# Performance work log

Measured on AMD Instinct MI355X. Metric: run time of the kernel, lower is better.

## Reference

```python
import jax, jax.numpy as jnp
import numpy as np

N_EMBD = 1024
N_HEAD = 16
HEAD_DIM = N_EMBD // N_HEAD


def setup_inputs() -> dict:
    key = jax.random.key(0)
    kx, kq, kk, kv, kp = jax.random.split(key, 5)
    B, S = 4, 2048
    x = jax.random.normal(kx, (B, S, N_EMBD), dtype=jnp.float32)
    # nn.Linear(n, n, bias=False): weight [out, in], y = x @ W.T
    s = 1.0 / np.sqrt(N_EMBD)
    Wq = jax.random.uniform(kq, (N_EMBD, N_EMBD), jnp.float32, -s, s)
    Wk = jax.random.uniform(kk, (N_EMBD, N_EMBD), jnp.float32, -s, s)
    Wv = jax.random.uniform(kv, (N_EMBD, N_EMBD), jnp.float32, -s, s)
    Wo = jax.random.uniform(kp, (N_EMBD, N_EMBD), jnp.float32, -s, s)
    return {"x": x, "Wq": Wq, "Wk": Wk, "Wv": Wv, "Wo": Wo}


def _split_heads(t):
    B, S, _ = t.shape
    return t.reshape(B, S, N_HEAD, HEAD_DIM).transpose(0, 2, 1, 3)  # [B,H,S,D]


def reference(x, Wq, Wk, Wv, Wo):
    q = _split_heads(x @ Wq.T)
    k = _split_heads(x @ Wk.T)
    v = _split_heads(x @ Wv.T)
    scale = 1.0 / np.sqrt(HEAD_DIM)
    scores = jnp.einsum('bhqd,bhkd->bhqk', q, k) * scale  # [B,H,S,S]
    S = x.shape[1]
    mask = jnp.tril(jnp.ones((S, S), dtype=bool))
    masked = jnp.where(mask[None, None], scores, -jnp.inf)
    attn = jax.nn.softmax(masked, axis=-1)
    heads = jnp.einsum('bhqk,bhkd->bhqd', attn, v)
    merged = heads.transpose(0, 2, 1, 3).reshape(x.shape[0], S, N_EMBD)
    return merged @ Wo.T
```

## Files before the change

### kernel.cpp

```cpp
#include <hip/hip_runtime.h>
#include <hip/hip_bf16.h>

typedef __hip_bfloat16 bf16;
typedef __attribute__((ext_vector_type(8))) short short8;
typedef __attribute__((ext_vector_type(4))) float f32x4;
typedef unsigned int uint32;

#define MFMA16(a, b, c) __builtin_amdgcn_mfma_f32_16x16x32_bf16(a, b, c, 0, 0, 0)

constexpr int EMB   = 1024;
constexpr int SEQ   = 2048;
constexpr int BATCH = 4;
constexpr int NH    = 16;
constexpr int HD    = 64;
constexpr int QKVW  = 3 * EMB;
constexpr float QSCALE = 0.125f * 1.44269504f;

__device__ __forceinline__ void gl_lds16(const bf16* g, bf16* l) {
    __builtin_amdgcn_global_load_lds(
        (const __attribute__((address_space(1))) void*)g,
        (__attribute__((address_space(3))) void*)l,
        16, 0, 0);
}

__device__ __forceinline__ float fexp2(float x) {
#if __has_builtin(__builtin_amdgcn_exp2f)
    return __builtin_amdgcn_exp2f(x);
#else
    return exp2f(x);
#endif
}

__device__ __forceinline__ uint32 pack2(float a, float b) {
    uint32 ua = __builtin_bit_cast(uint32, a) + 0x8000u;
    uint32 ub = __builtin_bit_cast(uint32, b) + 0x8000u;
    return __builtin_amdgcn_perm(ub, ua, 0x07060302u);
}

__device__ __forceinline__ bf16 fbf16(float f) {
    unsigned short u =
        (unsigned short)((__builtin_bit_cast(uint32, f) + 0x8000u) >> 16);
    return __builtin_bit_cast(bf16, u);
}

__device__ __forceinline__ int ps_dw(int row, int cd) {
    return row * 64 + ((((cd >> 2) ^ (row & 7)) << 3) + ((cd & 3) << 1));
}

__global__ void convert_all(const float* __restrict__ x,
                            const float* __restrict__ wq,
                            const float* __restrict__ wk,
                            const float* __restrict__ wv,
                            const float* __restrict__ wo,
                            bf16* __restrict__ xc,
                            bf16* __restrict__ wqkv,
                            bf16* __restrict__ woc) {
    const int NX = BATCH * SEQ * EMB;
    const int NW = EMB * EMB;
    const float* src; bf16* dst; int n4, b0, nb;
    const int blk = blockIdx.x;
    if (blk < 2048)      { src = x;  dst = xc;          n4 = NX / 4; b0 = 0;    nb = 2048; }
    else if (blk < 2304) { src = wq; dst = wqkv;        n4 = NW / 4; b0 = 2048; nb = 256; }
    else if (blk < 2560) { src = wk; dst = wqkv + NW;   n4 = NW / 4; b0 = 2304; nb = 256; }
    else if (blk < 2816) { src = wv; dst = wqkv + 2*NW; n4 = NW / 4; b0 = 2560; nb = 256; }
    else                 { src = wo; dst = woc;         n4 = NW / 4; b0 = 2816; nb = 256; }
    for (int i = (blk - b0) * 256 + threadIdx.x; i < n4; i += nb * 256) {
        float4 v = ((const float4*)src)[i];
        uint2 o;
        o.x = pack2(v.x, v.y);
        o.y = pack2(v.z, v.w);
        ((uint2*)dst)[i] = o;
    }
}

template <typename OutT>
__global__ __launch_bounds__(256) void gemm_bt(const bf16* __restrict__ A,
                                               const bf16* __restrict__ B,
                                               OutT* __restrict__ C,
                                               int M, int N, int K,
                                               float oscale, int qlim) {
    __shared__ __align__(16) bf16 As[128 * 64];
    __shared__ __align__(16) bf16 Bs[128 * 64];

    const int t    = threadIdx.x;
    const int lane = t & 63;
    const int wid  = t >> 6;
    const int l16  = lane & 15;
    const int quad = lane >> 4;
    const int e    = l16 & 7;
    const int wm   = (wid >> 1) * 64;
    const int wn   = (wid & 1) * 64;

    const int nwg = (int)gridDim.x;
    const int cpx = nwg >> 3;
    const int wg  = ((int)blockIdx.x & 7) * cpx + ((int)blockIdx.x >> 3);
    const int gx  = N >> 7;
    const int m0  = (wg / gx) * 128;
    const int n0  = (wg % gx) * 128;
    const float sc = (n0 < qlim) ? oscale : 1.0f;

    f32x4 acc[4][4] = {};
    const int srow = lane >> 3;
    const int scol = ((lane & 7) ^ srow) * 8;

    for (int k0 = 0; k0 < K; k0 += 64) {
        #pragma unroll
        for (int it = 0; it < 4; ++it) {
            int rb = it * 32 + wid * 8;
            gl_lds16(&A[(size_t)(m0 + rb + srow) * K + k0 + scol], &As[rb * 64]);
            gl_lds16(&B[(size_t)(n0 + rb + srow) * K + k0 + scol], &Bs[rb * 64]);
        }
        __syncthreads();
        #pragma unroll
        for (int ks = 0; ks < 64; ks += 32) {
            const int cb = (ks >> 3) + quad;
            short8 af[4], bfr[4];
            #pragma unroll
            for (int i = 0; i < 4; ++i)
                af[i] = *(const short8*)&As[(wm + i * 16 + l16) * 64 + ((cb ^ e) * 8)];
            #pragma unroll
            for (int j = 0; j < 4; ++j)
                bfr[j] = *(const short8*)&Bs[(wn + j * 16 + l16) * 64 + ((cb ^ e) * 8)];
            #pragma unroll
            for (int i = 0; i < 4; ++i)
                #pragma unroll
                for (int j = 0; j < 4; ++j)
                    acc[i][j] = MFMA16(af[i], bfr[j], acc[i][j]);
        }
        __syncthreads();
    }

    #pragma unroll
    for (int i = 0; i < 4; ++i)
        #pragma unroll
        for (int j = 0; j < 4; ++j)
            #pragma unroll
            for (int r = 0; r < 4; ++r) {
                int row = m0 + wm + i * 16 + quad * 4 + r;
                int col = n0 + wn + j * 16 + l16;
                float v = acc[i][j][r] * sc;
                if constexpr (sizeof(OutT) == 2)
                    C[(size_t)row * N + col] = fbf16(v);
                else
                    C[(size_t)row * N + col] = (OutT)v;
            }
}

__global__ __launch_bounds__(256) void transpose_v(const bf16* __restrict__ QKV,
                                                   bf16* __restrict__ Vt) {
    __shared__ __align__(16) bf16 Ts[4096];
    const int t  = threadIdx.x;
    const int st = blockIdx.x;
    const int bh = blockIdx.y;
    const int b  = bh >> 4, h = bh & 15;
    const int s0 = st * 64;

    const bf16* src = QKV + ((size_t)(b * SEQ + s0)) * QKVW + 2 * EMB + h * HD;
    {
        int r = t >> 3, cq = t & 7;
        #pragma unroll
        for (int it = 0; it < 2; ++it, r += 32) {
            uint4 v = *(const uint4*)&src[(size_t)r * QKVW + cq * 8];
            int blk = cq ^ (r >> 3);
            *(uint4*)&Ts[r * 64 + blk * 8] = v;
        }
    }
    __syncthreads();
    bf16* dst = Vt + (size_t)bh * HD * SEQ + s0;
    {
        int d = t >> 3;
        const int sq = t & 7;
        #pragma unroll
        for (int it = 0; it < 2; ++it, d += 32) {
            short8 ov;
            #pragma unroll
            for (int i = 0; i < 8; ++i) {
                int s = sq * 8 + i;
                ov[i] = (short)__bfloat16_as_ushort(
                    Ts[s * 64 + (((d >> 3) ^ sq) << 3) + (d & 7)]);
            }
            *(short8*)&dst[(size_t)d * SEQ + sq * 8] = ov;
        }
    }
}

__global__ __launch_bounds__(256) void flash_attn(const bf16* __restrict__ QKV,
                                                  const bf16* __restrict__ Vt,
                                                  bf16* __restrict__ O) {
    __shared__ __align__(16) bf16 Ks[2][64 * 64];
    __shared__ __align__(16) bf16 VTs[2][64 * 64];
    __shared__ __align__(16) bf16 Ps[4][16 * 64];

    const int t    = threadIdx.x;
    const int lane = t & 63;
    const int w    = t >> 6;
    const int l16  = lane & 15;
    const int quad = lane >> 4;
    const int e    = l16 & 7;

    const int lin = (int)blockIdx.x;
    const int wg  = ((lin & 7) << 7) + (lin >> 3);
    const int bh  = wg >> 4;
    const int pr  = wg & 15;
    const int b   = bh >> 4, h = bh & 15;

    const bf16* Qp = QKV + (size_t)b * SEQ * QKVW + h * HD;
    const bf16* Kp = QKV + (size_t)b * SEQ * QKVW + EMB + h * HD;
    const bf16* Vp = Vt + (size_t)bh * HD * SEQ;
    bf16* Op = O + (size_t)b * SEQ * EMB + h * HD;

    const int srow = lane >> 3;
    const int scol = ((lane & 7) ^ srow) * 8;

    auto stage = [&](int kt, int buf) {
        const int kbase = kt * 64;
        #pragma unroll
        for (int it = 0; it < 2; ++it) {
            int rb = it * 32 + w * 8;
            gl_lds16(&Kp[(size_t)(kbase + rb + srow) * QKVW + scol], &Ks[buf][rb * 64]);
            gl_lds16(&Vp[(size_t)(rb + srow) * SEQ + kbase + scol], &VTs[buf][rb * 64]);
        }
    };

    for (int pass = 0; pass < 2; ++pass) {
        const int qt = pass ? pr : 31 - pr;
        const int q0 = qt * 64;
        const int wq0 = q0 + w * 16;

        short8 bQ[2];
        {
            const size_t qr = (size_t)(wq0 + l16) * QKVW;
            bQ[0] = *(const short8*)&Qp[qr + quad * 8];
            bQ[1] = *(const short8*)&Qp[qr + 32 + quad * 8];
        }

        f32x4 o[4] = {};
        float lrow = 0.f;

        const int ntiles = qt + 1;

        stage(0, 0);
        if (ntiles > 1) stage(1, 1);

        for (int kt = 0; kt < ntiles; ++kt) {
            const int cur = kt & 1;
            const int kbase = kt * 64;
            if (kt < ntiles - 1) __builtin_amdgcn_s_waitcnt(0x0F74);
            else                 __builtin_amdgcn_s_waitcnt(0x0F70);
            __builtin_amdgcn_s_barrier();

            f32x4 sa[4];
            #pragma unroll
            for (int j = 0; j < 4; ++j) {
                f32x4 acc = {};
                acc = MFMA16(*(const short8*)&Ks[cur][(j * 16 + l16) * 64 + ((quad ^ e) * 8)],
                             bQ[0], acc);
                acc = MFMA16(*(const short8*)&Ks[cur][(j * 16 + l16) * 64 + (((4 + quad) ^ e) * 8)],
                             bQ[1], acc);
                sa[j] = acc;
            }

            float lsum = 0.f;
            if (kbase + 63 > wq0) {
                #pragma unroll
                for (int j = 0; j < 4; ++j)
                    #pragma unroll
                    for (int pp = 0; pp < 2; ++pp) {
                        int kg = kbase + j * 16 + quad * 4 + 2 * pp;
                        float e0 = fexp2(sa[j][2 * pp]);
                        float e1 = fexp2(sa[j][2 * pp + 1]);
                        float p0 = (kg     <= wq0 + l16) ? e0 : 0.f;
                        float p1 = (kg + 1 <= wq0 + l16) ? e1 : 0.f;
                        lsum += p0 + p1;
                        *(uint32*)&Ps[w][ps_dw(l16, j * 8 + quad * 2 + pp)] = pack2(p0, p1);
                    }
            } else {
                #pragma unroll
                for (int j = 0; j < 4; ++j)
                    #pragma unroll
                    for (int pp = 0; pp < 2; ++pp) {
                        float p0 = fexp2(sa[j][2 * pp]);
                        float p1 = fexp2(sa[j][2 * pp + 1]);
                        lsum += p0 + p1;
                        *(uint32*)&Ps[w][ps_dw(l16, j * 8 + quad * 2 + pp)] = pack2(p0, p1);
                    }
            }
            lrow += lsum;

            #pragma unroll
            for (int ks = 0; ks < 2; ++ks) {
                short8 bP = *(const short8*)&Ps[w][l16 * 64 + (((ks * 4 + quad) ^ e) << 3)];
                #pragma unroll
                for (int dg = 0; dg < 4; ++dg)
                    o[dg] = MFMA16(
                        *(const short8*)&VTs[cur][(dg * 16 + l16) * 64 + (((ks * 4 + quad) ^ e) * 8)],
                        bP, o[dg]);
            }

            __builtin_amdgcn_s_barrier();
            if (kt + 2 < ntiles) stage(kt + 2, cur);
        }

        {
            float l = lrow;
            l += __shfl_xor(l, 16);
            l += __shfl_xor(l, 32);
            float rl = 1.0f / l;
            #pragma unroll
            for (int dg = 0; dg < 4; ++dg)
                #pragma unroll
                for (int pp = 0; pp < 2; ++pp) {
                    float v0 = o[dg][2 * pp] * rl;
                    float v1 = o[dg][2 * pp + 1] * rl;
                    *(uint32*)&Ps[w][ps_dw(l16, dg * 8 + quad * 2 + pp)] = pack2(v0, v1);
                }
            #pragma unroll
            for (int it = 0; it < 2; ++it) {
                int qr = lane >> 2;
                int ch = (lane & 3) + 4 * it;
                short8 vv = *(const short8*)&Ps[w][qr * 64 + ((ch ^ (qr & 7)) << 3)];
                *(short8*)&Op[(size_t)(wq0 + qr) * EMB + ch * 8] = vv;
            }
        }
    }
}

extern "C" void kernel_launch(void* const* d_in, const int* in_sizes, int n_in,
                              void* d_out, int out_size, void* d_ws, size_t ws_size,
                              hipStream_t stream) {
    const float* x  = (const float*)d_in[0];
    const float* Wq = (const float*)d_in[1];
    const float* Wk = (const float*)d_in[2];
    const float* Wv = (const float*)d_in[3];
    const float* Wo = (const float*)d_in[4];
    float* out = (float*)d_out;
    bf16*  ws  = (bf16*)d_ws;

    const int M  = BATCH * SEQ;
    const int NX = M * EMB;
    const int NW = EMB * EMB;

    bf16* xc   = ws;
    bf16* Ab   = xc;
    bf16* Wqkv = ws + (size_t)NX;
    bf16* Woc  = Wqkv + 3 * (size_t)NW;
    bf16* QKV  = Woc + NW;
    bf16* Vt   = QKV + (size_t)M * QKVW;

    convert_all<<<3072, 256, 0, stream>>>(x, Wq, Wk, Wv, Wo, xc, Wqkv, Woc);

    gemm_bt<bf16><<<dim3((QKVW / 128) * (M / 128)), 256, 0, stream>>>(
        xc, Wqkv, QKV, M, QKVW, EMB, QSCALE, EMB);

    transpose_v<<<dim3(SEQ / 64, BATCH * NH), 256, 0, stream>>>(QKV, Vt);

    flash_attn<<<dim3((SEQ / 64 / 2) * BATCH * NH), 256, 0, stream>>>(QKV, Vt, Ab);

    gemm_bt<float><<<dim3((EMB / 128) * (M / 128)), 256, 0, stream>>>(
        Ab, Woc, out, M, EMB, EMB, 1.0f, 0);
}
```

Baseline: 257.3 us.

## Double-buffer GEMM LDS tiles with async global-to-LDS prefetch and XCD tile remap

The bf16 GEMM now keeps two LDS buffers for A and B. It prefetches the tile two steps ahead with global_load_lds, using explicit vmcnt waits and barriers in place of __syncthreads, so loads overlap with the MFMA work. It also changes how workgroups map to tiles: each XCD gets a contiguous band of M rows and walks N tiles, aiming for better L2 reuse. The cost is double the LDS use (64KB), which may lower occupancy, plus reliance on hand-encoded waitcnt values being correct.

```diff
diff --git a/kernel.cpp b/kernel.cpp
--- a/kernel.cpp
+++ b/kernel.cpp
@@ -79,8 +79,8 @@
                                                OutT* __restrict__ C,
                                                int M, int N, int K,
                                                float oscale, int qlim) {
-    __shared__ __align__(16) bf16 As[128 * 64];
-    __shared__ __align__(16) bf16 Bs[128 * 64];
+    __shared__ __align__(16) bf16 As[2][128 * 64];
+    __shared__ __align__(16) bf16 Bs[2][128 * 64];
 
     const int t    = threadIdx.x;
     const int lane = t & 63;
@@ -91,43 +91,59 @@
     const int wm   = (wid >> 1) * 64;
     const int wn   = (wid & 1) * 64;
 
-    const int nwg = (int)gridDim.x;
-    const int cpx = nwg >> 3;
-    const int wg  = ((int)blockIdx.x & 7) * cpx + ((int)blockIdx.x >> 3);
-    const int gx  = N >> 7;
-    const int m0  = (wg / gx) * 128;
-    const int n0  = (wg % gx) * 128;
-    const float sc = (n0 < qlim) ? oscale : 1.0f;
+    const int nwg   = (int)gridDim.x;
+    const int cpx   = nwg >> 3;
+    const int gx    = N >> 7;
+    const int mrows = cpx / gx;
+    const int xcd   = (int)blockIdx.x & 7;
+    const int local = (int)blockIdx.x >> 3;
+    const int m0    = (xcd * mrows + (local % mrows)) * 128;
+    const int n0    = (local / mrows) * 128;
+    const float sc  = (n0 < qlim) ? oscale : 1.0f;
 
     f32x4 acc[4][4] = {};
     const int srow = lane >> 3;
     const int scol = ((lane & 7) ^ srow) * 8;
 
-    for (int k0 = 0; k0 < K; k0 += 64) {
+    auto stage = [&](int kt, int buf) {
+        const int k0 = kt * 64;
         #pragma unroll
         for (int it = 0; it < 4; ++it) {
             int rb = it * 32 + wid * 8;
-            gl_lds16(&A[(size_t)(m0 + rb + srow) * K + k0 + scol], &As[rb * 64]);
-            gl_lds16(&B[(size_t)(n0 + rb + srow) * K + k0 + scol], &Bs[rb * 64]);
-        }
-        __syncthreads();
+            gl_lds16(&A[(size_t)(m0 + rb + srow) * K + k0 + scol], &As[buf][rb * 64]);
+            gl_lds16(&B[(size_t)(n0 + rb + srow) * K + k0 + scol], &Bs[buf][rb * 64]);
+        }
+    };
+
+    const int nk = K >> 6;
+    stage(0, 0);
+    stage(1, 1);
+
+    for (int kt = 0; kt < nk; ++kt) {
+        const int cur = kt & 1;
+        if (kt < nk - 1) __builtin_amdgcn_s_waitcnt(0x0F78);
+        else             __builtin_amdgcn_s_waitcnt(0x0F70);
+        __builtin_amdgcn_s_barrier();
+
         #pragma unroll
         for (int ks = 0; ks < 64; ks += 32) {
             const int cb = (ks >> 3) + quad;
             short8 af[4], bfr[4];
             #pragma unroll
             for (int i = 0; i < 4; ++i)
-                af[i] = *(const short8*)&As[(wm + i * 16 + l16) * 64 + ((cb ^ e) * 8)];
+                af[i] = *(const short8*)&As[cur][(wm + i * 16 + l16) * 64 + ((cb ^ e) * 8)];
             #pragma unroll
             for (int j = 0; j < 4; ++j)
-                bfr[j] = *(const short8*)&Bs[(wn + j * 16 + l16) * 64 + ((cb ^ e) * 8)];
+                bfr[j] = *(const short8*)&Bs[cur][(wn + j * 16 + l16) * 64 + ((cb ^ e) * 8)];
             #pragma unroll
             for (int i = 0; i < 4; ++i)
                 #pragma unroll
                 for (int j = 0; j < 4; ++j)
                     acc[i][j] = MFMA16(af[i], bfr[j], acc[i][j]);
         }
-        __syncthreads();
+
+        __builtin_amdgcn_s_barrier();
+        if (kt + 2 < nk) stage(kt + 2, cur);
     }
 
     #pragma unroll
```

Result: faster. 237.9 us (-7.5%).
